# Kernel optimization log

Hardware: AMD Instinct MI355X
Metric: run time of the kernel (lower is better)

Reference implementation:

```python
import jax, jax.numpy as jnp
import numpy as np

SCALE = 20.0
EPS = 1e-8  # torch F.cosine_similarity eps

def _l2norm(x):
    n = jnp.sqrt(jnp.sum(x * x, axis=-1, keepdims=True))
    return x / jnp.maximum(n, EPS)

def setup_inputs() -> dict:
    key = jax.random.key(0)
    k1, k2, k3 = jax.random.split(key, 3)
    B, D, N = 4096, 1024, 4096
    return {
        "query_embeddings": jax.random.normal(k1, (B, D), dtype=jnp.float32),
        "positive_embeddings": jax.random.normal(k2, (B, D), dtype=jnp.float32),
        "negative_embeddings": jax.random.normal(k3, (N, D), dtype=jnp.float32),
    }

def reference(query_embeddings, positive_embeddings, negative_embeddings):
    B = query_embeddings.shape[0]
    q = _l2norm(query_embeddings)                      # (B, D)
    docs = jnp.concatenate([positive_embeddings, negative_embeddings], axis=0)
    d = _l2norm(docs)                                  # (B+N, D)
    scores = SCALE * jnp.einsum("bd,cd->bc", q, d)     # (B, B+N)
    labels = jnp.arange(B)
    logp = jax.nn.log_softmax(scores, axis=-1)
    loss = -jnp.mean(jnp.take_along_axis(logp, labels[:, None], axis=1))
    return loss
```

## Files before the change

kernel.cpp:

```cpp
#include <hip/hip_runtime.h>
#include <stdint.h>

typedef __attribute__((ext_vector_type(8))) short s16x8;
typedef __attribute__((ext_vector_type(4))) float f32x4;

#define DIM 1024
#define NQ 4096
#define NDOC 8192
#define NKT 16

__device__ __forceinline__ unsigned f2bf(float f) {
    unsigned int u = __builtin_bit_cast(unsigned int, f);
    u += 0x7FFFu + ((u >> 16) & 1u);
    return u >> 16;
}
__device__ __forceinline__ float bf2f(unsigned int s) {
    unsigned int u = (s & 0xFFFFu) << 16;
    return __builtin_bit_cast(float, u);
}

__global__ __launch_bounds__(256) void normalize_kernel(
    const float* __restrict__ q, const float* __restrict__ pos,
    const float* __restrict__ neg, unsigned short* __restrict__ qn,
    unsigned short* __restrict__ dn, float* __restrict__ rowsum) {
    int row = blockIdx.x * 4 + (threadIdx.x >> 6);
    int lane = threadIdx.x & 63;
    const float* src;
    unsigned short* dst;
    if (row < 4096) {
        src = q + (size_t)row * DIM; dst = qn + (size_t)row * DIM;
        if (lane == 0) rowsum[row] = 0.f;
    } else if (row < 8192) {
        src = pos + (size_t)(row - 4096) * DIM; dst = dn + (size_t)(row - 4096) * DIM;
    } else {
        src = neg + (size_t)(row - 8192) * DIM; dst = dn + (size_t)(row - 4096) * DIM;
    }
    float4 v[4];
    float ss = 0.f;
#pragma unroll
    for (int it = 0; it < 4; ++it) {
        v[it] = reinterpret_cast<const float4*>(src)[it * 64 + lane];
        ss += v[it].x * v[it].x + v[it].y * v[it].y + v[it].z * v[it].z + v[it].w * v[it].w;
    }
#pragma unroll
    for (int off = 32; off > 0; off >>= 1) ss += __shfl_xor(ss, off, 64);
    float inv = rsqrtf(ss);
#pragma unroll
    for (int it = 0; it < 4; ++it) {
        uint2 o;
        o.x = f2bf(v[it].x * inv) | (f2bf(v[it].y * inv) << 16);
        o.y = f2bf(v[it].z * inv) | (f2bf(v[it].w * inv) << 16);
        reinterpret_cast<uint2*>(dst)[it * 64 + lane] = o;
    }
}

#define GLOAD_LDS(g, l) __builtin_amdgcn_global_load_lds( \
    (const __attribute__((address_space(1))) void*)(g),   \
    (__attribute__((address_space(3))) void*)(l), 16, 0, 0)

#define STG(kt, r, bufByte) {                                                     \
    GLOAD_LDS(aG + (r) * 65536 + (kt) * 64, ldsc + (bufByte) + ((r) * 512 + tid) * 16); \
    GLOAD_LDS(bG + (r) * 65536 + (kt) * 64, ldsc + (bufByte) + 32768 + ((r) * 512 + tid) * 16); \
  }

#define PHASE(CUR, KS, H, DOB, DOSTG, KT1, R) {                                   \
    if (DOB) {                                                                    \
        _Pragma("unroll") for (int n = 0; n < 4; ++n)                             \
            bF[n] = *(const s16x8*)(ldsc + (CUR) + (bB0 ^ ((KS) * 64)) + n * 2048); \
    }                                                                             \
    s16x8 aF[4];                                                                  \
    _Pragma("unroll") for (int m = 0; m < 4; ++m)                                 \
        aF[m] = *(const s16x8*)(ldsc + (CUR) + (aB0 ^ ((KS) * 64)) + ((H) * 64 + m * 16) * 128); \
    if (DOSTG) STG(KT1, R, (CUR) ^ 65536);                                        \
    __builtin_amdgcn_s_barrier();                                                 \
    __builtin_amdgcn_s_setprio(1);                                                \
    _Pragma("unroll") for (int m = 0; m < 4; ++m)                                 \
        _Pragma("unroll") for (int n = 0; n < 4; ++n)                             \
            acc[(H) * 4 + m][n] = __builtin_amdgcn_mfma_f32_16x16x32_bf16(        \
                aF[m], bF[n], acc[(H) * 4 + m][n], 0, 0, 0);                      \
    __builtin_amdgcn_s_setprio(0);                                                \
  }

__global__ __launch_bounds__(512, 2) void gemm_lse_kernel(
    const unsigned short* __restrict__ qn, const unsigned short* __restrict__ dn,
    float* __restrict__ rowsum) {
    extern __shared__ char ldsc[];
    const int tid = threadIdx.x;
    const int lane = tid & 63;
    const int wid = tid >> 6;
    const int wr = wid >> 2;
    const int wc = wid & 3;
    const int lr = lane & 15;
    const int lk = lane >> 4;

    int bid = blockIdx.x;
    int xcd = bid & 7, local = bid >> 3;
    int brow = (xcd >> 2) * 8 + (local >> 3);
    int bcol = (xcd & 3) * 8 + (local & 7);

    const int srow = tid >> 3;
    const int sslot = (tid & 7) ^ (srow & 7);
    const unsigned short* aG = qn + (size_t)(brow * 256 + srow) * DIM + sslot * 8;
    const unsigned short* bG = dn + (size_t)(bcol * 256 + srow) * DIM + sslot * 8;

    const int s0 = lk ^ (lane & 7);
    const int aB0 = (wr * 128 + lr) * 128 + s0 * 16;
    const int bB0 = 32768 + (wc * 64 + lr) * 128 + s0 * 16;

    f32x4 acc[8][4] = {};

#pragma unroll
    for (int r = 0; r < 4; ++r) STG(0, r, 0);
    STG(1, 0, 65536);
    asm volatile("s_waitcnt vmcnt(2)" ::: "memory");
    __builtin_amdgcn_s_barrier();

    for (int t = 0; t < NKT; ++t) {
        const int cur = (t & 1) ? 65536 : 0;
        const bool st = t < NKT - 1;
        s16x8 bF[4];
        PHASE(cur, 0, 0, true,  st, t + 1, 1)
        PHASE(cur, 0, 1, false, st, t + 1, 2)
        PHASE(cur, 1, 0, true,  st, t + 1, 3)
        PHASE(cur, 1, 1, false, false, 0, 0)
        if (t < NKT - 2) {
            __builtin_amdgcn_s_barrier();
            STG(t + 2, 0, cur);
            asm volatile("s_waitcnt vmcnt(2)" ::: "memory");
            __builtin_amdgcn_s_barrier();
        } else if (t == NKT - 2) {
            __builtin_amdgcn_s_barrier();
            asm volatile("s_waitcnt vmcnt(0)" ::: "memory");
            __builtin_amdgcn_s_barrier();
        }
    }

#pragma unroll
    for (int m = 0; m < 8; ++m) {
#pragma unroll
        for (int j = 0; j < 4; ++j) {
            float r = 0.f;
#pragma unroll
            for (int n = 0; n < 4; ++n) {
                float s = 20.f * acc[m][n][j] - 20.f;
                r += __expf(s);
            }
#pragma unroll
            for (int off = 1; off < 16; off <<= 1) r += __shfl_xor(r, off, 64);
            if (lr == 0) {
                int row = brow * 256 + wr * 128 + m * 16 + lk * 4 + j;
                atomicAdd(&rowsum[row], r);
            }
        }
    }
}

__global__ __launch_bounds__(256) void loss_kernel(
    const unsigned short* __restrict__ qn, const unsigned short* __restrict__ dn,
    const float* __restrict__ rowsum, float* __restrict__ rowloss) {
    int row = blockIdx.x * 4 + (threadIdx.x >> 6);
    int lane = threadIdx.x & 63;
    const uint4* a4 = reinterpret_cast<const uint4*>(qn + (size_t)row * DIM);
    const uint4* b4 = reinterpret_cast<const uint4*>(dn + (size_t)row * DIM);
    float s = 0.f;
#pragma unroll
    for (int it = 0; it < 2; ++it) {
        uint4 ua = a4[it * 64 + lane], ub = b4[it * 64 + lane];
        s += bf2f(ua.x) * bf2f(ub.x) + bf2f(ua.x >> 16) * bf2f(ub.x >> 16);
        s += bf2f(ua.y) * bf2f(ub.y) + bf2f(ua.y >> 16) * bf2f(ub.y >> 16);
        s += bf2f(ua.z) * bf2f(ub.z) + bf2f(ua.z >> 16) * bf2f(ub.z >> 16);
        s += bf2f(ua.w) * bf2f(ub.w) + bf2f(ua.w >> 16) * bf2f(ub.w >> 16);
    }
#pragma unroll
    for (int off = 32; off > 0; off >>= 1) s += __shfl_xor(s, off, 64);
    if (lane == 0)
        rowloss[row] = (20.f + __logf(rowsum[row])) - 20.f * s;
}

__global__ __launch_bounds__(1024) void reduce_kernel(
    const float* __restrict__ rowloss, float* __restrict__ out) {
    int t = threadIdx.x;
    float s = 0.f;
#pragma unroll
    for (int i = 0; i < 4; ++i) s += rowloss[t + i * 1024];
#pragma unroll
    for (int off = 32; off > 0; off >>= 1) s += __shfl_xor(s, off, 64);
    __shared__ float wsum[16];
    if ((t & 63) == 0) wsum[t >> 6] = s;
    __syncthreads();
    if (t == 0) {
        float tot = 0.f;
#pragma unroll
        for (int i = 0; i < 16; ++i) tot += wsum[i];
        out[0] = tot * (1.f / 4096.f);
    }
}

extern "C" void kernel_launch(void* const* d_in, const int* in_sizes, int n_in,
                              void* d_out, int out_size, void* d_ws, size_t ws_size,
                              hipStream_t stream) {
    const float* q   = (const float*)d_in[0];
    const float* pos = (const float*)d_in[1];
    const float* neg = (const float*)d_in[2];
    float* out = (float*)d_out;
    char* ws = (char*)d_ws;
    unsigned short* qn = (unsigned short*)ws;
    unsigned short* dn = (unsigned short*)(ws + (size_t)8 * 1024 * 1024);
    float* rowsum  = (float*)(ws + (size_t)24 * 1024 * 1024);
    float* rowloss = (float*)(ws + (size_t)24 * 1024 * 1024 + 16384);

    static bool attr_set = false;
    if (!attr_set) {
        (void)hipFuncSetAttribute((const void*)gemm_lse_kernel,
                                  hipFuncAttributeMaxDynamicSharedMemorySize, 131072);
        attr_set = true;
    }

    normalize_kernel<<<3072, 256, 0, stream>>>(q, pos, neg, qn, dn, rowsum);
    gemm_lse_kernel<<<512, 512, 131072, stream>>>(qn, dn, rowsum);
    loss_kernel<<<1024, 256, 0, stream>>>(qn, dn, rowsum, rowloss);
    reduce_kernel<<<1, 1024, 0, stream>>>(rowloss, out);
}
```

Baseline: 171.3 us.

## Switch GEMM to FP8 scaled MFMA and fuse diagonal extraction into GEMM

Normalized embeddings are now stored as FP8 instead of bf16, and the GEMM uses the 16x16x128 scaled f8f6f4 MFMA with half as many K iterations. The positive-pair score is taken from the GEMM accumulators on diagonal tiles, which removes the separate loss kernel, and the final reduction is folded into one finalize kernel. FP8 halves memory traffic and doubles the MFMA rate, at the cost of accuracy in the scores and loss. Launch bounds drop from two blocks per CU to one.

```diff
diff --git a/kernel.cpp b/kernel.cpp
--- a/kernel.cpp
+++ b/kernel.cpp
@@ -1,39 +1,29 @@
 #include <hip/hip_runtime.h>
 #include <stdint.h>
 
-typedef __attribute__((ext_vector_type(8))) short s16x8;
+typedef __attribute__((ext_vector_type(8))) int i32x8;
 typedef __attribute__((ext_vector_type(4))) float f32x4;
 
 #define DIM 1024
 #define NQ 4096
 #define NDOC 8192
-#define NKT 16
-
-__device__ __forceinline__ unsigned f2bf(float f) {
-    unsigned int u = __builtin_bit_cast(unsigned int, f);
-    u += 0x7FFFu + ((u >> 16) & 1u);
-    return u >> 16;
-}
-__device__ __forceinline__ float bf2f(unsigned int s) {
-    unsigned int u = (s & 0xFFFFu) << 16;
-    return __builtin_bit_cast(float, u);
-}
+#define NKT 8
 
 __global__ __launch_bounds__(256) void normalize_kernel(
     const float* __restrict__ q, const float* __restrict__ pos,
-    const float* __restrict__ neg, unsigned short* __restrict__ qn,
-    unsigned short* __restrict__ dn, float* __restrict__ rowsum) {
+    const float* __restrict__ neg, uint8_t* __restrict__ qn8,
+    uint8_t* __restrict__ dn8, float* __restrict__ rowsum) {
     int row = blockIdx.x * 4 + (threadIdx.x >> 6);
     int lane = threadIdx.x & 63;
     const float* src;
-    unsigned short* dst;
+    uint8_t* dst;
     if (row < 4096) {
-        src = q + (size_t)row * DIM; dst = qn + (size_t)row * DIM;
+        src = q + (size_t)row * DIM; dst = qn8 + (size_t)row * DIM;
         if (lane == 0) rowsum[row] = 0.f;
     } else if (row < 8192) {
-        src = pos + (size_t)(row - 4096) * DIM; dst = dn + (size_t)(row - 4096) * DIM;
+        src = pos + (size_t)(row - 4096) * DIM; dst = dn8 + (size_t)(row - 4096) * DIM;
     } else {
-        src = neg + (size_t)(row - 8192) * DIM; dst = dn + (size_t)(row - 4096) * DIM;
+        src = neg + (size_t)(row - 8192) * DIM; dst = dn8 + (size_t)(row - 4096) * DIM;
     }
     float4 v[4];
     float ss = 0.f;
@@ -47,10 +37,9 @@
     float inv = rsqrtf(ss);
 #pragma unroll
     for (int it = 0; it < 4; ++it) {
-        uint2 o;
-        o.x = f2bf(v[it].x * inv) | (f2bf(v[it].y * inv) << 16);
-        o.y = f2bf(v[it].z * inv) | (f2bf(v[it].w * inv) << 16);
-        reinterpret_cast<uint2*>(dst)[it * 64 + lane] = o;
+        int b = __builtin_amdgcn_cvt_pk_fp8_f32(v[it].x * inv, v[it].y * inv, 0, false);
+        b = __builtin_amdgcn_cvt_pk_fp8_f32(v[it].z * inv, v[it].w * inv, b, true);
+        *reinterpret_cast<unsigned*>(dst + it * 256 + lane * 4) = (unsigned)b;
     }
 }
 
@@ -58,32 +47,23 @@
     (const __attribute__((address_space(1))) void*)(g),   \
     (__attribute__((address_space(3))) void*)(l), 16, 0, 0)
 
-#define STG(kt, r, bufByte) {                                                     \
-    GLOAD_LDS(aG + (r) * 65536 + (kt) * 64, ldsc + (bufByte) + ((r) * 512 + tid) * 16); \
-    GLOAD_LDS(bG + (r) * 65536 + (kt) * 64, ldsc + (bufByte) + 32768 + ((r) * 512 + tid) * 16); \
+#define STG2(bufByte, kt, r) {                                              \
+    GLOAD_LDS(aG + (r) * 65536 + (kt) * 128, ldsc + (bufByte) + ((r) * 512 + tid) * 16); \
+    GLOAD_LDS(bG + (r) * 65536 + (kt) * 128, ldsc + (bufByte) + 32768 + ((r) * 512 + tid) * 16); \
   }
 
-#define PHASE(CUR, KS, H, DOB, DOSTG, KT1, R) {                                   \
-    if (DOB) {                                                                    \
-        _Pragma("unroll") for (int n = 0; n < 4; ++n)                             \
-            bF[n] = *(const s16x8*)(ldsc + (CUR) + (bB0 ^ ((KS) * 64)) + n * 2048); \
-    }                                                                             \
-    s16x8 aF[4];                                                                  \
-    _Pragma("unroll") for (int m = 0; m < 4; ++m)                                 \
-        aF[m] = *(const s16x8*)(ldsc + (CUR) + (aB0 ^ ((KS) * 64)) + ((H) * 64 + m * 16) * 128); \
-    if (DOSTG) STG(KT1, R, (CUR) ^ 65536);                                        \
-    __builtin_amdgcn_s_barrier();                                                 \
-    __builtin_amdgcn_s_setprio(1);                                                \
-    _Pragma("unroll") for (int m = 0; m < 4; ++m)                                 \
-        _Pragma("unroll") for (int n = 0; n < 4; ++n)                             \
-            acc[(H) * 4 + m][n] = __builtin_amdgcn_mfma_f32_16x16x32_bf16(        \
-                aF[m], bF[n], acc[(H) * 4 + m][n], 0, 0, 0);                      \
-    __builtin_amdgcn_s_setprio(0);                                                \
-  }
-
-__global__ __launch_bounds__(512, 2) void gemm_lse_kernel(
-    const unsigned short* __restrict__ qn, const unsigned short* __restrict__ dn,
-    float* __restrict__ rowsum) {
+__device__ __forceinline__ i32x8 pack8(int4 lo, int4 hi) {
+    i32x8 v;
+    v[0] = lo.x; v[1] = lo.y; v[2] = lo.z; v[3] = lo.w;
+    v[4] = hi.x; v[5] = hi.y; v[6] = hi.z; v[7] = hi.w;
+    return v;
+}
+
+#define SC1 0x7F7F7F7F
+
+__global__ __launch_bounds__(512, 1) void gemm_lse_kernel(
+    const uint8_t* __restrict__ qn8, const uint8_t* __restrict__ dn8,
+    float* __restrict__ rowsum, float* __restrict__ diag) {
     extern __shared__ char ldsc[];
     const int tid = threadIdx.x;
     const int lane = tid & 63;
@@ -100,32 +80,67 @@
 
     const int srow = tid >> 3;
     const int sslot = (tid & 7) ^ (srow & 7);
-    const unsigned short* aG = qn + (size_t)(brow * 256 + srow) * DIM + sslot * 8;
-    const unsigned short* bG = dn + (size_t)(bcol * 256 + srow) * DIM + sslot * 8;
-
-    const int s0 = lk ^ (lane & 7);
-    const int aB0 = (wr * 128 + lr) * 128 + s0 * 16;
-    const int bB0 = 32768 + (wc * 64 + lr) * 128 + s0 * 16;
+    const uint8_t* aG = qn8 + (size_t)(brow * 256 + srow) * DIM + sslot * 16;
+    const uint8_t* bG = dn8 + (size_t)(bcol * 256 + srow) * DIM + sslot * 16;
+
+    const int s0 = ((lk * 2) ^ (lane & 7)) * 16;
+    const int aB0 = (wr * 128 + lr) * 128 + s0;
+    const int bB0 = 32768 + (wc * 64 + lr) * 128 + s0;
 
     f32x4 acc[8][4] = {};
 
 #pragma unroll
-    for (int r = 0; r < 4; ++r) STG(0, r, 0);
-    STG(1, 0, 65536);
+    for (int r = 0; r < 4; ++r) STG2(0, 0, r);
+    STG2(65536, 1, 0);
     asm volatile("s_waitcnt vmcnt(2)" ::: "memory");
     __builtin_amdgcn_s_barrier();
 
     for (int t = 0; t < NKT; ++t) {
         const int cur = (t & 1) ? 65536 : 0;
+        const int nxt = cur ^ 65536;
         const bool st = t < NKT - 1;
-        s16x8 bF[4];
-        PHASE(cur, 0, 0, true,  st, t + 1, 1)
-        PHASE(cur, 0, 1, false, st, t + 1, 2)
-        PHASE(cur, 1, 0, true,  st, t + 1, 3)
-        PHASE(cur, 1, 1, false, false, 0, 0)
+        i32x8 bV[4], aV[4];
+#pragma unroll
+        for (int n = 0; n < 4; ++n) {
+            int4 lo = *(const int4*)(ldsc + cur + bB0 + n * 2048);
+            int4 hi = *(const int4*)(ldsc + cur + (bB0 ^ 16) + n * 2048);
+            bV[n] = pack8(lo, hi);
+        }
+#pragma unroll
+        for (int m = 0; m < 4; ++m) {
+            int4 lo = *(const int4*)(ldsc + cur + aB0 + m * 2048);
+            int4 hi = *(const int4*)(ldsc + cur + (aB0 ^ 16) + m * 2048);
+            aV[m] = pack8(lo, hi);
+        }
+        if (st) { STG2(nxt, t + 1, 1); STG2(nxt, t + 1, 2); }
+        __builtin_amdgcn_s_barrier();
+        __builtin_amdgcn_s_setprio(1);
+#pragma unroll
+        for (int m = 0; m < 4; ++m)
+#pragma unroll
+            for (int n = 0; n < 4; ++n)
+                acc[m][n] = __builtin_amdgcn_mfma_scale_f32_16x16x128_f8f6f4(
+                    aV[m], bV[n], acc[m][n], 0, 0, 0, SC1, 0, SC1);
+        __builtin_amdgcn_s_setprio(0);
+#pragma unroll
+        for (int m = 0; m < 4; ++m) {
+            int4 lo = *(const int4*)(ldsc + cur + aB0 + (m + 4) * 2048);
+            int4 hi = *(const int4*)(ldsc + cur + (aB0 ^ 16) + (m + 4) * 2048);
+            aV[m] = pack8(lo, hi);
+        }
+        if (st) STG2(nxt, t + 1, 3);
+        __builtin_amdgcn_s_barrier();
+        __builtin_amdgcn_s_setprio(1);
+#pragma unroll
+        for (int m = 0; m < 4; ++m)
+#pragma unroll
+            for (int n = 0; n < 4; ++n)
+                acc[m + 4][n] = __builtin_amdgcn_mfma_scale_f32_16x16x128_f8f6f4(
+                    aV[m], bV[n], acc[m + 4][n], 0, 0, 0, SC1, 0, SC1);
+        __builtin_amdgcn_s_setprio(0);
         if (t < NKT - 2) {
             __builtin_amdgcn_s_barrier();
-            STG(t + 2, 0, cur);
+            STG2(cur, t + 2, 0);
             asm volatile("s_waitcnt vmcnt(2)" ::: "memory");
             __builtin_amdgcn_s_barrier();
         } else if (t == NKT - 2) {
@@ -153,36 +168,30 @@
             }
         }
     }
-}
-
-__global__ __launch_bounds__(256) void loss_kernel(
-    const unsigned short* __restrict__ qn, const unsigned short* __restrict__ dn,
-    const float* __restrict__ rowsum, float* __restrict__ rowloss) {
-    int row = blockIdx.x * 4 + (threadIdx.x >> 6);
-    int lane = threadIdx.x & 63;
-    const uint4* a4 = reinterpret_cast<const uint4*>(qn + (size_t)row * DIM);
-    const uint4* b4 = reinterpret_cast<const uint4*>(dn + (size_t)row * DIM);
-    float s = 0.f;
-#pragma unroll
-    for (int it = 0; it < 2; ++it) {
-        uint4 ua = a4[it * 64 + lane], ub = b4[it * 64 + lane];
-        s += bf2f(ua.x) * bf2f(ub.x) + bf2f(ua.x >> 16) * bf2f(ub.x >> 16);
-        s += bf2f(ua.y) * bf2f(ub.y) + bf2f(ua.y >> 16) * bf2f(ub.y >> 16);
-        s += bf2f(ua.z) * bf2f(ub.z) + bf2f(ua.z >> 16) * bf2f(ub.z >> 16);
-        s += bf2f(ua.w) * bf2f(ub.w) + bf2f(ua.w >> 16) * bf2f(ub.w >> 16);
-    }
-#pragma unroll
-    for (int off = 32; off > 0; off >>= 1) s += __shfl_xor(s, off, 64);
-    if (lane == 0)
-        rowloss[row] = (20.f + __logf(rowsum[row])) - 20.f * s;
-}
-
-__global__ __launch_bounds__(1024) void reduce_kernel(
-    const float* __restrict__ rowloss, float* __restrict__ out) {
+    if (brow == bcol) {
+#pragma unroll
+        for (int m = 0; m < 8; ++m)
+#pragma unroll
+            for (int j = 0; j < 4; ++j) {
+                int tr = wr * 128 + m * 16 + lk * 4 + j;
+#pragma unroll
+                for (int n = 0; n < 4; ++n)
+                    if (wc * 64 + n * 16 + lr == tr)
+                        diag[brow * 256 + tr] = 20.f * acc[m][n][j];
+            }
+    }
+}
+
+__global__ __launch_bounds__(1024) void finalize_kernel(
+    const float* __restrict__ rowsum, const float* __restrict__ diag,
+    float* __restrict__ out) {
     int t = threadIdx.x;
     float s = 0.f;
 #pragma unroll
-    for (int i = 0; i < 4; ++i) s += rowloss[t + i * 1024];
+    for (int i = 0; i < 4; ++i) {
+        int r = t + i * 1024;
+        s += (20.f + __logf(rowsum[r])) - diag[r];
+    }
 #pragma unroll
     for (int off = 32; off > 0; off >>= 1) s += __shfl_xor(s, off, 64);
     __shared__ float wsum[16];
@@ -204,10 +213,10 @@
     const float* neg = (const float*)d_in[2];
     float* out = (float*)d_out;
     char* ws = (char*)d_ws;
-    unsigned short* qn = (unsigned short*)ws;
-    unsigned short* dn = (unsigned short*)(ws + (size_t)8 * 1024 * 1024);
-    float* rowsum  = (float*)(ws + (size_t)24 * 1024 * 1024);
-    float* rowloss = (float*)(ws + (size_t)24 * 1024 * 1024 + 16384);
+    uint8_t* qn8 = (uint8_t*)ws;
+    uint8_t* dn8 = (uint8_t*)(ws + (size_t)4 * 1024 * 1024);
+    float* rowsum = (float*)(ws + (size_t)12 * 1024 * 1024);
+    float* diag   = (float*)(ws + (size_t)12 * 1024 * 1024 + 16384);
 
     static bool attr_set = false;
     if (!attr_set) {
@@ -216,8 +225,7 @@
         attr_set = true;
     }
 
-    normalize_kernel<<<3072, 256, 0, stream>>>(q, pos, neg, qn, dn, rowsum);
-    gemm_lse_kernel<<<512, 512, 131072, stream>>>(qn, dn, rowsum);
-    loss_kernel<<<1024, 256, 0, stream>>>(qn, dn, rowsum, rowloss);
-    reduce_kernel<<<1, 1024, 0, stream>>>(rowloss, out);
-}
+    normalize_kernel<<<3072, 256, 0, stream>>>(q, pos, neg, qn8, dn8, rowsum);
+    gemm_lse_kernel<<<512, 512, 131072, stream>>>(qn8, dn8, rowsum, diag);
+    finalize_kernel<<<1, 1024, 0, stream>>>(rowsum, diag, out);
+}
```

After: 451.7 us. 164% more time.

## Use 16 waves per GEMM block and fuse diagonal extraction into GEMM epilogue

Applied to the files above, without the earlier changes.

The GEMM block grows from 8 to 16 waves. Each wave now computes a 64x64 sub-tile instead of 128x64, which halves the accumulator registers per wave, and staging now loads two row chunks per call. The separate loss kernel that recomputed the positive dot products is removed: diagonal-tile blocks write the scaled diagonal score directly, and a single finalize kernel combines log-sum and diagonal. This drops one launch and a re-read of the normalized matrices, but with 1024 threads per block the barriers become heavier and only one block may fit per CU given the 128KB LDS.

```diff
diff --git a/kernel.cpp b/kernel.cpp
--- a/kernel.cpp
+++ b/kernel.cpp
@@ -13,10 +13,6 @@
     unsigned int u = __builtin_bit_cast(unsigned int, f);
     u += 0x7FFFu + ((u >> 16) & 1u);
     return u >> 16;
-}
-__device__ __forceinline__ float bf2f(unsigned int s) {
-    unsigned int u = (s & 0xFFFFu) << 16;
-    return __builtin_bit_cast(float, u);
 }
 
 __global__ __launch_bounds__(256) void normalize_kernel(
@@ -58,32 +54,30 @@
     (const __attribute__((address_space(1))) void*)(g),   \
     (__attribute__((address_space(3))) void*)(l), 16, 0, 0)
 
-#define STG(kt, r, bufByte) {                                                     \
-    GLOAD_LDS(aG + (r) * 65536 + (kt) * 64, ldsc + (bufByte) + ((r) * 512 + tid) * 16); \
-    GLOAD_LDS(bG + (r) * 65536 + (kt) * 64, ldsc + (bufByte) + 32768 + ((r) * 512 + tid) * 16); \
+#define STG2(bufByte, kt, r) {                                                        \
+    GLOAD_LDS(aG + (r) * 131072 + (kt) * 64, ldsc + (bufByte) + ((r) * 1024 + tid) * 16); \
+    GLOAD_LDS(bG + (r) * 131072 + (kt) * 64, ldsc + (bufByte) + 32768 + ((r) * 1024 + tid) * 16); \
   }
 
-#define PHASE(CUR, KS, H, DOB, DOSTG, KT1, R) {                                   \
-    if (DOB) {                                                                    \
-        _Pragma("unroll") for (int n = 0; n < 4; ++n)                             \
-            bF[n] = *(const s16x8*)(ldsc + (CUR) + (bB0 ^ ((KS) * 64)) + n * 2048); \
-    }                                                                             \
-    s16x8 aF[4];                                                                  \
+#define PHASE(CUR, KS, DOSTG, KT1) {                                              \
+    s16x8 bF[4], aF[4];                                                           \
+    _Pragma("unroll") for (int n = 0; n < 4; ++n)                                 \
+        bF[n] = *(const s16x8*)(ldsc + (CUR) + (bB0 ^ ((KS) * 64)) + n * 2048);   \
     _Pragma("unroll") for (int m = 0; m < 4; ++m)                                 \
-        aF[m] = *(const s16x8*)(ldsc + (CUR) + (aB0 ^ ((KS) * 64)) + ((H) * 64 + m * 16) * 128); \
-    if (DOSTG) STG(KT1, R, (CUR) ^ 65536);                                        \
+        aF[m] = *(const s16x8*)(ldsc + (CUR) + (aB0 ^ ((KS) * 64)) + m * 2048);   \
+    if (DOSTG) STG2((CUR) ^ 65536, KT1, 1);                                       \
     __builtin_amdgcn_s_barrier();                                                 \
     __builtin_amdgcn_s_setprio(1);                                                \
     _Pragma("unroll") for (int m = 0; m < 4; ++m)                                 \
         _Pragma("unroll") for (int n = 0; n < 4; ++n)                             \
-            acc[(H) * 4 + m][n] = __builtin_amdgcn_mfma_f32_16x16x32_bf16(        \
-                aF[m], bF[n], acc[(H) * 4 + m][n], 0, 0, 0);                      \
+            acc[m][n] = __builtin_amdgcn_mfma_f32_16x16x32_bf16(                  \
+                aF[m], bF[n], acc[m][n], 0, 0, 0);                                \
     __builtin_amdgcn_s_setprio(0);                                                \
   }
 
-__global__ __launch_bounds__(512, 2) void gemm_lse_kernel(
+__global__ __launch_bounds__(1024, 4) void gemm_lse_kernel(
     const unsigned short* __restrict__ qn, const unsigned short* __restrict__ dn,
-    float* __restrict__ rowsum) {
+    float* __restrict__ rowsum, float* __restrict__ diag) {
     extern __shared__ char ldsc[];
     const int tid = threadIdx.x;
     const int lane = tid & 63;
@@ -104,28 +98,24 @@
     const unsigned short* bG = dn + (size_t)(bcol * 256 + srow) * DIM + sslot * 8;
 
     const int s0 = lk ^ (lane & 7);
-    const int aB0 = (wr * 128 + lr) * 128 + s0 * 16;
+    const int aB0 = (wr * 64 + lr) * 128 + s0 * 16;
     const int bB0 = 32768 + (wc * 64 + lr) * 128 + s0 * 16;
 
-    f32x4 acc[8][4] = {};
-
-#pragma unroll
-    for (int r = 0; r < 4; ++r) STG(0, r, 0);
-    STG(1, 0, 65536);
+    f32x4 acc[4][4] = {};
+
+    STG2(0, 0, 0); STG2(0, 0, 1);
+    STG2(65536, 1, 0);
     asm volatile("s_waitcnt vmcnt(2)" ::: "memory");
     __builtin_amdgcn_s_barrier();
 
     for (int t = 0; t < NKT; ++t) {
         const int cur = (t & 1) ? 65536 : 0;
         const bool st = t < NKT - 1;
-        s16x8 bF[4];
-        PHASE(cur, 0, 0, true,  st, t + 1, 1)
-        PHASE(cur, 0, 1, false, st, t + 1, 2)
-        PHASE(cur, 1, 0, true,  st, t + 1, 3)
-        PHASE(cur, 1, 1, false, false, 0, 0)
+        PHASE(cur, 0, st, t + 1)
+        PHASE(cur, 1, false, 0)
         if (t < NKT - 2) {
             __builtin_amdgcn_s_barrier();
-            STG(t + 2, 0, cur);
+            STG2(cur, t + 2, 0);
             asm volatile("s_waitcnt vmcnt(2)" ::: "memory");
             __builtin_amdgcn_s_barrier();
         } else if (t == NKT - 2) {
@@ -136,7 +126,7 @@
     }
 
 #pragma unroll
-    for (int m = 0; m < 8; ++m) {
+    for (int m = 0; m < 4; ++m) {
 #pragma unroll
         for (int j = 0; j < 4; ++j) {
             float r = 0.f;
@@ -148,41 +138,35 @@
 #pragma unroll
             for (int off = 1; off < 16; off <<= 1) r += __shfl_xor(r, off, 64);
             if (lr == 0) {
-                int row = brow * 256 + wr * 128 + m * 16 + lk * 4 + j;
+                int row = brow * 256 + wr * 64 + m * 16 + lk * 4 + j;
                 atomicAdd(&rowsum[row], r);
             }
         }
     }
-}
-
-__global__ __launch_bounds__(256) void loss_kernel(
-    const unsigned short* __restrict__ qn, const unsigned short* __restrict__ dn,
-    const float* __restrict__ rowsum, float* __restrict__ rowloss) {
-    int row = blockIdx.x * 4 + (threadIdx.x >> 6);
-    int lane = threadIdx.x & 63;
-    const uint4* a4 = reinterpret_cast<const uint4*>(qn + (size_t)row * DIM);
-    const uint4* b4 = reinterpret_cast<const uint4*>(dn + (size_t)row * DIM);
-    float s = 0.f;
-#pragma unroll
-    for (int it = 0; it < 2; ++it) {
-        uint4 ua = a4[it * 64 + lane], ub = b4[it * 64 + lane];
-        s += bf2f(ua.x) * bf2f(ub.x) + bf2f(ua.x >> 16) * bf2f(ub.x >> 16);
-        s += bf2f(ua.y) * bf2f(ub.y) + bf2f(ua.y >> 16) * bf2f(ub.y >> 16);
-        s += bf2f(ua.z) * bf2f(ub.z) + bf2f(ua.z >> 16) * bf2f(ub.z >> 16);
-        s += bf2f(ua.w) * bf2f(ub.w) + bf2f(ua.w >> 16) * bf2f(ub.w >> 16);
-    }
-#pragma unroll
-    for (int off = 32; off > 0; off >>= 1) s += __shfl_xor(s, off, 64);
-    if (lane == 0)
-        rowloss[row] = (20.f + __logf(rowsum[row])) - 20.f * s;
-}
-
-__global__ __launch_bounds__(1024) void reduce_kernel(
-    const float* __restrict__ rowloss, float* __restrict__ out) {
+    if (brow == bcol) {
+#pragma unroll
+        for (int m = 0; m < 4; ++m)
+#pragma unroll
+            for (int j = 0; j < 4; ++j) {
+                int tr = wr * 64 + m * 16 + lk * 4 + j;
+#pragma unroll
+                for (int n = 0; n < 4; ++n)
+                    if (wc * 64 + n * 16 + lr == tr)
+                        diag[brow * 256 + tr] = 20.f * acc[m][n][j];
+            }
+    }
+}
+
+__global__ __launch_bounds__(1024) void finalize_kernel(
+    const float* __restrict__ rowsum, const float* __restrict__ diag,
+    float* __restrict__ out) {
     int t = threadIdx.x;
     float s = 0.f;
 #pragma unroll
-    for (int i = 0; i < 4; ++i) s += rowloss[t + i * 1024];
+    for (int i = 0; i < 4; ++i) {
+        int r = t + i * 1024;
+        s += (20.f + __logf(rowsum[r])) - diag[r];
+    }
 #pragma unroll
     for (int off = 32; off > 0; off >>= 1) s += __shfl_xor(s, off, 64);
     __shared__ float wsum[16];
@@ -206,8 +190,8 @@
     char* ws = (char*)d_ws;
     unsigned short* qn = (unsigned short*)ws;
     unsigned short* dn = (unsigned short*)(ws + (size_t)8 * 1024 * 1024);
-    float* rowsum  = (float*)(ws + (size_t)24 * 1024 * 1024);
-    float* rowloss = (float*)(ws + (size_t)24 * 1024 * 1024 + 16384);
+    float* rowsum = (float*)(ws + (size_t)24 * 1024 * 1024);
+    float* diag   = (float*)(ws + (size_t)24 * 1024 * 1024 + 16384);
 
     static bool attr_set = false;
     if (!attr_set) {
@@ -217,7 +201,6 @@
     }
 
     normalize_kernel<<<3072, 256, 0, stream>>>(q, pos, neg, qn, dn, rowsum);
-    gemm_lse_kernel<<<512, 512, 131072, stream>>>(qn, dn, rowsum);
-    loss_kernel<<<1024, 256, 0, stream>>>(qn, dn, rowsum, rowloss);
-    reduce_kernel<<<1, 1024, 0, stream>>>(rowloss, out);
-}
+    gemm_lse_kernel<<<512, 1024, 131072, stream>>>(qn, dn, rowsum, diag);
+    finalize_kernel<<<1, 1024, 0, stream>>>(rowsum, diag, out);
+}
```

Result: faster. 163.5 us (-4.6%).
